# Kernel optimization log

Measured on AMD Instinct MI355X. Metric: run time of the kernel, lower is better.

Reference implementation:

```python
import jax, jax.numpy as jnp
from jax import lax
import numpy as np

HID = 64      # lstm hidden / gat in-dim
HEADS = 4
DH = HID // HEADS  # 16 per-head dim
OUT = 3       # horizon


def setup_inputs() -> dict:
    key = jax.random.key(0)
    ks = jax.random.split(key, 18)
    B, T, N = 8, 12, 1500
    p = lambda k, shape: jax.random.normal(k, shape, jnp.float32) * 0.1
    return {
        "x": jax.random.normal(ks[0], (B, T, N), jnp.float32),
        "adj": jax.random.randint(ks[1], (N, N), 0, 2, jnp.int32),
        "lstm_Wih0": p(ks[2], (4 * HID, 1)),
        "lstm_Whh0": p(ks[3], (4 * HID, HID)),
        "lstm_bih0": p(ks[4], (4 * HID,)),
        "lstm_bhh0": p(ks[5], (4 * HID,)),
        "lstm_Wih1": p(ks[6], (4 * HID, HID)),
        "lstm_Whh1": p(ks[7], (4 * HID, HID)),
        "lstm_bih1": p(ks[8], (4 * HID,)),
        "lstm_bhh1": p(ks[9], (4 * HID,)),
        "gat0_W": p(ks[10], (HID, HID)),
        "gat0_asrc": p(ks[11], (HEADS, DH)),
        "gat0_adst": p(ks[12], (HEADS, DH)),
        "gat1_W": p(ks[13], (HID, HID)),
        "gat1_asrc": p(ks[14], (HEADS, DH)),
        "gat1_adst": p(ks[15], (HEADS, DH)),
        "out_W": p(ks[16], (OUT, HID)),
        "out_b": p(ks[17], (OUT,)),
    }


def _lstm_layer(seq, Wih, Whh, bih, bhh):
    # seq: (T, BN, in) -> (T, BN, H). PyTorch gate order i,f,g,o.
    BN = seq.shape[1]
    H = Whh.shape[1]

    def step(carry, xt):
        h, c = carry
        g = xt @ Wih.T + h @ Whh.T + bih + bhh
        i, f, gg, o = jnp.split(g, 4, axis=-1)
        c = jax.nn.sigmoid(f) * c + jax.nn.sigmoid(i) * jnp.tanh(gg)
        h = jax.nn.sigmoid(o) * jnp.tanh(c)
        return (h, c), h

    zero = jnp.zeros((BN, H), seq.dtype)
    _, hs = lax.scan(step, (zero, zero), seq)
    return hs


def _gat(h_in, W, asrc, adst, mask):
    # h_in: (B,N,HID); mask: (1,N,N,1) bool
    B, N, _ = h_in.shape
    Hn, D = asrc.shape
    hp = (h_in @ W.T).reshape(B, N, Hn, D)           # (B,N,H,D)
    e_src = jnp.einsum('bnhd,hd->bnh', hp, asrc)
    e_dst = jnp.einsum('bnhd,hd->bnh', hp, adst)
    e = e_src[:, :, None, :] + e_dst[:, None, :, :]   # (B,i,j,H)
    e = jnp.where(e > 0, e, 0.2 * e)                  # LeakyReLU(0.2)
    e = jnp.where(mask, e, -jnp.inf)
    alpha = jax.nn.softmax(e, axis=2)                 # softmax over neighbors j
    ho = jnp.einsum('bijh,bjhd->bihd', alpha, hp)
    return ho.reshape(B, N, Hn * D)


def reference(x, adj, lstm_Wih0, lstm_Whh0, lstm_bih0, lstm_bhh0,
              lstm_Wih1, lstm_Whh1, lstm_bih1, lstm_bhh1,
              gat0_W, gat0_asrc, gat0_adst, gat1_W, gat1_asrc, gat1_adst,
              out_W, out_b):
    B, T, N = x.shape
    # (B,T,N) -> (B*N, T, 1) -> time-major (T, B*N, 1)
    xf = jnp.transpose(x, (0, 2, 1)).reshape(B * N, T, 1)
    seq = jnp.transpose(xf, (1, 0, 2))
    hs = _lstm_layer(seq, lstm_Wih0, lstm_Whh0, lstm_bih0, lstm_bhh0)
    hs = _lstm_layer(hs, lstm_Wih1, lstm_Whh1, lstm_bih1, lstm_bhh1)
    h = hs[-1].reshape(B, N, HID)                     # last-step hidden of top layer
    mask = (adj > 0)[None, :, :, None]
    h = jax.nn.relu(_gat(h, gat0_W, gat0_asrc, gat0_adst, mask))
    h = jax.nn.relu(_gat(h, gat1_W, gat1_asrc, gat1_adst, mask))
    out = h @ out_W.T + out_b                         # (B,N,OUT)
    return jnp.transpose(out, (0, 2, 1))              # (B,OUT,N)
```

## Files before the change

### kernel.cpp

```cpp
#include <hip/hip_runtime.h>
#include <hip/hip_bf16.h>


#define BN 12000
#define NNODE 1500
#define NB 8
#define TT 12
#define NPAD 1536
#define LOG2E 1.44269504f

typedef __bf16 bf16x8 __attribute__((ext_vector_type(8)));
typedef __bf16 bf16x4 __attribute__((ext_vector_type(4)));
typedef float  f32x4  __attribute__((ext_vector_type(4)));

__device__ __forceinline__ float rcpf(float v) { return __builtin_amdgcn_rcpf(v); }
__device__ __forceinline__ float exp2f_(float v) { return __builtin_amdgcn_exp2f(v); }
__device__ __forceinline__ float sigf(float v) { return rcpf(1.f + __expf(-v)); }
__device__ __forceinline__ float tanhf_(float v) {
    return fmaf(2.f, rcpf(1.f + __expf(-2.f * v)), -1.f);
}

__device__ __forceinline__ int hp_idx(int b, int head, int jc) {
    return (((b << 2) + head) * 48 + jc) << 9;
}

__device__ __forceinline__ bf16x8 ldcvt(const float* p) {
    f32x4 a = *(const f32x4*)p;
    f32x4 b = *(const f32x4*)(p + 4);
    bf16x8 r;
    #pragma unroll
    for (int i = 0; i < 4; ++i) { r[i] = (__bf16)a[i]; r[4 + i] = (__bf16)b[i]; }
    return r;
}

__global__ __launch_bounds__(512, 1) void lstm_mask_prep(
    const float* __restrict__ x,
    const float* __restrict__ Wih0, const float* __restrict__ Whh0,
    const float* __restrict__ bih0, const float* __restrict__ bhh0,
    const float* __restrict__ Wih1, const float* __restrict__ Whh1,
    const float* __restrict__ bih1, const float* __restrict__ bhh1,
    const int* __restrict__ adj, unsigned int* __restrict__ mask,
    const float* __restrict__ gW, const float* __restrict__ asrc,
    const float* __restrict__ adst,
    __bf16* __restrict__ hpT, float* __restrict__ esT, float* __restrict__ edT)
{
    if (blockIdx.x >= 750) {
        int wid  = (blockIdx.x - 750) * 8 + (threadIdx.x >> 6);
        int lane = threadIdx.x & 63;
        #pragma unroll 4
        for (int u = 0; u < 16; ++u) {
            int task = wid * 16 + u;
            int i = task / 24, ch = task - i * 24;
            int j = ch * 64 + lane;
            int a = (i < NNODE && j < NNODE) ? adj[i * NNODE + j] : 0;
            unsigned long long m = __ballot(a > 0);
            if (lane == 0 && i < 1504) *(unsigned long long*)&mask[i * 48 + ch * 2] = m;
        }
        return;
    }

    __shared__ __align__(16) __bf16 h0s[16 * 72];
    __shared__ __align__(16) __bf16 h1s[16 * 72];
    __shared__ __align__(16) float  xls[TT * 16];
    __shared__ float avs[128];
    __shared__ __align__(16) __bf16 hp_t[64 * 24];

    int tid  = threadIdx.x;
    int w    = __builtin_amdgcn_readfirstlane(tid >> 6);
    int lane = tid & 63;
    int l15  = lane & 15;
    int qd   = lane >> 4;
    bool lo  = l15 < 8;
    int dloc = l15 & 7;
    int d    = 8 * w + dloc;

    for (int e = tid; e < (16 * 72) / 2; e += 512) ((unsigned int*)h1s)[e] = 0u;
    if (tid < TT * 16) {
        int t = tid >> 4, m = tid & 15;
        int s = blockIdx.x * 16 + m;
        int bb = s / NNODE, nn = s - bb * NNODE;
        xls[tid] = x[bb * (TT * NNODE) + t * NNODE + nn];
    }
    if (tid < 64)       avs[tid] = asrc[tid] * LOG2E;
    else if (tid < 128) avs[tid] = adst[tid - 64] * LOG2E;

    int gA = (lo ? 0 : 64) + d;
    int gB = (lo ? 128 : 192) + d;
    bf16x8 B0A[2], B0B[2], B1A[4], B1B[4];
    #pragma unroll
    for (int kt = 0; kt < 2; ++kt) {
        B0A[kt] = ldcvt(&Whh0[gA * 64 + 32 * kt + 8 * qd]);
        B0B[kt] = ldcvt(&Whh0[gB * 64 + 32 * kt + 8 * qd]);
        B1A[kt] = ldcvt(&Wih1[gA * 64 + 32 * kt + 8 * qd]);
        B1B[kt] = ldcvt(&Wih1[gB * 64 + 32 * kt + 8 * qd]);
        B1A[kt + 2] = ldcvt(&Whh1[gA * 64 + 32 * kt + 8 * qd]);
        B1B[kt + 2] = ldcvt(&Whh1[gB * 64 + 32 * kt + 8 * qd]);
    }
    float b0A = bih0[gA] + bhh0[gA], b0B = bih0[gB] + bhh0[gB];
    float b1A = bih1[gA] + bhh1[gA], b1B = bih1[gB] + bhh1[gB];
    float w0A = Wih0[gA], w0B = Wih0[gB];

    float pwi = Wih0[d],       pbi = bih0[d]       + bhh0[d];
    float pwg = Wih0[128 + d], pbg = bih0[128 + d] + bhh0[128 + d];
    float pwo = Wih0[192 + d], pbo = bih0[192 + d] + bhh0[192 + d];

    float c0[2], c1[2];
    c0[0] = c0[1] = c1[0] = c1[1] = 0.f;

    __syncthreads();

    #pragma unroll
    for (int rl = 0; rl < 2; ++rl) {
        int rr = lo ? rl : 2 + rl;
        int m = 4 * qd + rr;
        float xv = xls[m];
        float gi = fmaf(pwi, xv, pbi);
        float gg = fmaf(pwg, xv, pbg);
        float go = fmaf(pwo, xv, pbo);
        float c = sigf(gi) * tanhf_(gg);
        c0[rl] = c;
        h0s[m * 72 + d] = (__bf16)(sigf(go) * tanhf_(c));
    }
    __syncthreads();

    for (int t = 0; t < TT; ++t) {
        bool last = (t == TT - 1);
        bf16x8 a0[2], a1[2];
        #pragma unroll
        for (int kt = 0; kt < 2; ++kt) {
            a0[kt] = *(bf16x8*)&h0s[l15 * 72 + 32 * kt + 8 * qd];
            a1[kt] = *(bf16x8*)&h1s[l15 * 72 + 32 * kt + 8 * qd];
        }
        f32x4 AA1, AB1, AA0, AB0;
        #pragma unroll
        for (int r = 0; r < 4; ++r) { AA1[r] = b1A; AB1[r] = b1B; }
        if (!last) {
            f32x4 xv = *(f32x4*)&xls[(t + 1) * 16 + 4 * qd];
            #pragma unroll
            for (int r = 0; r < 4; ++r) {
                AA0[r] = fmaf(w0A, xv[r], b0A);
                AB0[r] = fmaf(w0B, xv[r], b0B);
            }
        }
        #pragma unroll
        for (int kt = 0; kt < 2; ++kt) {
            AA1 = __builtin_amdgcn_mfma_f32_16x16x32_bf16(a0[kt], B1A[kt], AA1, 0, 0, 0);
            AB1 = __builtin_amdgcn_mfma_f32_16x16x32_bf16(a0[kt], B1B[kt], AB1, 0, 0, 0);
            AA1 = __builtin_amdgcn_mfma_f32_16x16x32_bf16(a1[kt], B1A[kt + 2], AA1, 0, 0, 0);
            AB1 = __builtin_amdgcn_mfma_f32_16x16x32_bf16(a1[kt], B1B[kt + 2], AB1, 0, 0, 0);
        }
        if (!last) {
            #pragma unroll
            for (int kt = 0; kt < 2; ++kt) {
                AA0 = __builtin_amdgcn_mfma_f32_16x16x32_bf16(a0[kt], B0A[kt], AA0, 0, 0, 0);
                AB0 = __builtin_amdgcn_mfma_f32_16x16x32_bf16(a0[kt], B0B[kt], AB0, 0, 0, 0);
            }
        }
        __syncthreads();

        {
            float shA0 = __shfl_xor(lo ? AA1[2] : AA1[0], 8);
            float shA1 = __shfl_xor(lo ? AA1[3] : AA1[1], 8);
            float shB0 = __shfl_xor(lo ? AB1[2] : AB1[0], 8);
            float shB1 = __shfl_xor(lo ? AB1[3] : AB1[1], 8);
            #pragma unroll
            for (int rl = 0; rl < 2; ++rl) {
                int rr = lo ? rl : 2 + rl;
                float ownA = AA1[rr], ownB = AB1[rr];
                float shA = rl ? shA1 : shA0, shB = rl ? shB1 : shB0;
                float gi = lo ? ownA : shA;
                float gf = lo ? shA : ownA;
                float gg = lo ? ownB : shB;
                float go = lo ? shB : ownB;
                float c = sigf(gf) * c1[rl] + sigf(gi) * tanhf_(gg);
                c1[rl] = c;
                float hv = sigf(go) * tanhf_(c);
                int m = 4 * qd + rr;
                h1s[m * 72 + d] = (__bf16)hv;
            }
        }
        if (!last) {
            float shA0 = __shfl_xor(lo ? AA0[2] : AA0[0], 8);
            float shA1 = __shfl_xor(lo ? AA0[3] : AA0[1], 8);
            float shB0 = __shfl_xor(lo ? AB0[2] : AB0[0], 8);
            float shB1 = __shfl_xor(lo ? AB0[3] : AB0[1], 8);
            #pragma unroll
            for (int rl = 0; rl < 2; ++rl) {
                int rr = lo ? rl : 2 + rl;
                float ownA = AA0[rr], ownB = AB0[rr];
                float shA = rl ? shA1 : shA0, shB = rl ? shB1 : shB0;
                float gi = lo ? ownA : shA;
                float gf = lo ? shA : ownA;
                float gg = lo ? ownB : shB;
                float go = lo ? shB : ownB;
                float c = sigf(gf) * c0[rl] + sigf(gi) * tanhf_(gg);
                c0[rl] = c;
                int m = 4 * qd + rr;
                h0s[m * 72 + d] = (__bf16)(sigf(go) * tanhf_(c));
            }
        }
        __syncthreads();
    }

    int s0 = blockIdx.x * 16;
    if (w < 4) {
        int mt = w;
        bf16x8 Bf0 = *(bf16x8*)&h1s[l15 * 72 + 8 * qd];
        bf16x8 Bf1 = *(bf16x8*)&h1s[l15 * 72 + 32 + 8 * qd];
        bf16x8 A0 = ldcvt(&gW[(mt * 16 + l15) * 64 + 8 * qd]);
        bf16x8 A1 = ldcvt(&gW[(mt * 16 + l15) * 64 + 32 + 8 * qd]);
        f32x4 a = {0.f, 0.f, 0.f, 0.f};
        a = __builtin_amdgcn_mfma_f32_16x16x32_bf16(A0, Bf0, a, 0, 0, 0);
        a = __builtin_amdgcn_mfma_f32_16x16x32_bf16(A1, Bf1, a, 0, 0, 0);
        float ts = 0.f, td = 0.f;
        #pragma unroll
        for (int r = 0; r < 4; ++r) {
            int dd = mt * 16 + qd * 4 + r;
            ts = fmaf(a[r], avs[dd], ts);
            td = fmaf(a[r], avs[64 + dd], td);
            hp_t[dd * 24 + l15] = (__bf16)a[r];
        }
        ts += __shfl_xor(ts, 16); ts += __shfl_xor(ts, 32);
        td += __shfl_xor(td, 16); td += __shfl_xor(td, 32);
        if (qd == 0) {
            int s = s0 + l15, b = s / NNODE, n = s - b * NNODE;
            esT[(b * 4 + mt) * NPAD + n] = ts;
            edT[(b * 4 + mt) * NPAD + n] = td;
        }
    }
    __syncthreads();
    if (tid < 256) {
        int dim = tid >> 2, seg = tid & 3;
        int head = dim >> 4, dl = dim & 15;
        int b0 = s0 / NNODE, b1e = (s0 + 15) / NNODE;
        if (b0 == b1e) {
            int n0 = s0 - b0 * NNODE;
            int nj = n0 + seg * 4;
            int jc = nj >> 5, ko = nj & 31;
            bf16x4 v = *(bf16x4*)&hp_t[dim * 24 + seg * 4];
            *(bf16x4*)&hpT[hp_idx(b0, head, jc) + dl * 32 + ko] = v;
        } else {
            #pragma unroll
            for (int u = 0; u < 4; ++u) {
                int ss = s0 + seg * 4 + u;
                int b = ss / NNODE, n = ss - b * NNODE;
                hpT[hp_idx(b, head, n >> 5) + dl * 32 + (n & 31)] =
                    hp_t[dim * 24 + seg * 4 + u];
            }
        }
    }
}

__global__ __launch_bounds__(256, 1) void gat_mid(
    const __bf16* __restrict__ hpT, const float* __restrict__ esT,
    const float* __restrict__ edT, const unsigned int* __restrict__ mask,
    const float* __restrict__ gW, const float* __restrict__ asrc,
    const float* __restrict__ adst,
    __bf16* __restrict__ hpT1, float* __restrict__ esT1, float* __restrict__ edT1)
{
    __shared__ __align__(16) float edls[4 * NPAD];
    __shared__ unsigned int mskls[48 * 16];
    __shared__ float Ss[4][16];
    __shared__ float hbuf[16 * 72];
    __shared__ float avs[128];
    __shared__ __align__(16) __bf16 hp1_t[64 * 24];

    int tid  = threadIdx.x;
    int wv   = tid >> 6;
    int lane = tid & 63;
    int l15  = lane & 15;
    int qd   = lane >> 4;
    int b    = blockIdx.x / 94;
    int i0   = (blockIdx.x % 94) * 16;

    if (tid < 64)       avs[tid] = asrc[tid] * LOG2E;
    else if (tid < 128) avs[tid] = adst[tid - 64] * LOG2E;
    {
        const float4* src = (const float4*)(edT + (b * 4) * NPAD);
        float4* dst = (float4*)edls;
        for (int u = tid; u < NPAD; u += 256) dst[u] = src[u];
    }
    for (int u = tid; u < 16 * 48; u += 256) {
        int il = u / 48, c = u - il * 48;
        mskls[c * 16 + il] = mask[(i0 + il) * 48 + c];
    }
    __syncthreads();

    const __bf16* Bbase = hpT + hp_idx(b, wv, 0) + l15 * 32 + qd * 8;
    const float* edrow = edls + wv * NPAD;
    float esv = esT[(b * 4 + wv) * NPAD + i0 + l15];

    f32x4 acc = {0.f, 0.f, 0.f, 0.f};
    float S = 0.f;

    for (int jt = 0; jt < 12; ++jt) {
        #pragma unroll
        for (int kt = 0; kt < 4; ++kt) {
            int jc = jt * 4 + kt;
            int jk = jc * 32 + qd * 8;
            float4 e0 = *(const float4*)&edrow[jk];
            float4 e1 = *(const float4*)&edrow[jk + 4];
            unsigned int mb = (mskls[jc * 16 + l15] >> (qd * 8)) & 0xffu;
            float ej[8] = {e0.x, e0.y, e0.z, e0.w, e1.x, e1.y, e1.z, e1.w};
            bf16x8 A;
            #pragma unroll
            for (int jj = 0; jj < 8; ++jj) {
                float e = esv + ej[jj];
                e = fmaxf(e, 0.2f * e);
                float p = ((mb >> jj) & 1u) ? exp2f_(e) : 0.f;
                S += p;
                A[jj] = (__bf16)p;
            }
            bf16x8 B = *(const bf16x8*)(Bbase + (jc << 9));
            acc = __builtin_amdgcn_mfma_f32_16x16x32_bf16(A, B, acc, 0, 0, 0);
        }
    }

    S += __shfl_xor(S, 16);
    S += __shfl_xor(S, 32);
    if (qd == 0) Ss[wv][l15] = S;
    __syncthreads();

    #pragma unroll
    for (int r = 0; r < 4; ++r) {
        float rs = rcpf(Ss[wv][qd * 4 + r]);
        hbuf[(qd * 4 + r) * 72 + (wv << 4) + l15] = fmaxf(acc[r] * rs, 0.f);
    }
    __syncthreads();

    {
        int mt = wv;
        bf16x8 Bf0 = ldcvt(&hbuf[l15 * 72 + 8 * qd]);
        bf16x8 Bf1 = ldcvt(&hbuf[l15 * 72 + 32 + 8 * qd]);
        bf16x8 A0 = ldcvt(&gW[(mt * 16 + l15) * 64 + 8 * qd]);
        bf16x8 A1 = ldcvt(&gW[(mt * 16 + l15) * 64 + 32 + 8 * qd]);
        f32x4 a = {0.f, 0.f, 0.f, 0.f};
        a = __builtin_amdgcn_mfma_f32_16x16x32_bf16(A0, Bf0, a, 0, 0, 0);
        a = __builtin_amdgcn_mfma_f32_16x16x32_bf16(A1, Bf1, a, 0, 0, 0);
        float ts = 0.f, td = 0.f;
        #pragma unroll
        for (int r = 0; r < 4; ++r) {
            int dd = mt * 16 + qd * 4 + r;
            ts = fmaf(a[r], avs[dd], ts);
            td = fmaf(a[r], avs[64 + dd], td);
            hp1_t[dd * 24 + l15] = (__bf16)a[r];
        }
        ts += __shfl_xor(ts, 16); ts += __shfl_xor(ts, 32);
        td += __shfl_xor(td, 16); td += __shfl_xor(td, 32);
        if (qd == 0) {
            int n = i0 + l15;
            esT1[(b * 4 + mt) * NPAD + n] = ts;
            edT1[(b * 4 + mt) * NPAD + n] = td;
        }
    }
    __syncthreads();
    {
        int dim = tid >> 2, seg = tid & 3;
        int head = dim >> 4, dl = dim & 15;
        int nn0 = i0 + seg * 4;
        int jc = nn0 >> 5, ko = nn0 & 31;
        bf16x4 v = *(bf16x4*)&hp1_t[dim * 24 + seg * 4];
        *(bf16x4*)&hpT1[hp_idx(b, head, jc) + dl * 32 + ko] = v;
    }
}

__global__ __launch_bounds__(256, 1) void gat_fin(
    const __bf16* __restrict__ hpT, const float* __restrict__ esT,
    const float* __restrict__ edT, const unsigned int* __restrict__ mask,
    const float* __restrict__ oW, const float* __restrict__ ob,
    float* __restrict__ outp)
{
    __shared__ __align__(16) float edls[4 * NPAD];
    __shared__ unsigned int mskls[48 * 16];
    __shared__ float Ss[4][16];
    __shared__ float hbuf[16 * 72];
    __shared__ float oWs[192];
    __shared__ float obs[3];

    int tid  = threadIdx.x;
    int wv   = tid >> 6;
    int lane = tid & 63;
    int l15  = lane & 15;
    int qd   = lane >> 4;
    int b    = blockIdx.x / 94;
    int i0   = (blockIdx.x % 94) * 16;

    if (tid < 192) oWs[tid] = oW[tid];
    if (tid < 3)   obs[tid] = ob[tid];
    {
        const float4* src = (const float4*)(edT + (b * 4) * NPAD);
        float4* dst = (float4*)edls;
        for (int u = tid; u < NPAD; u += 256) dst[u] = src[u];
    }
    for (int u = tid; u < 16 * 48; u += 256) {
        int il = u / 48, c = u - il * 48;
        mskls[c * 16 + il] = mask[(i0 + il) * 48 + c];
    }
    __syncthreads();

    const __bf16* Bbase = hpT + hp_idx(b, wv, 0) + l15 * 32 + qd * 8;
    const float* edrow = edls + wv * NPAD;
    float esv = esT[(b * 4 + wv) * NPAD + i0 + l15];

    f32x4 acc = {0.f, 0.f, 0.f, 0.f};
    float S = 0.f;

    for (int jt = 0; jt < 12; ++jt) {
        #pragma unroll
        for (int kt = 0; kt < 4; ++kt) {
            int jc = jt * 4 + kt;
            int jk = jc * 32 + qd * 8;
            float4 e0 = *(const float4*)&edrow[jk];
            float4 e1 = *(const float4*)&edrow[jk + 4];
            unsigned int mb = (mskls[jc * 16 + l15] >> (qd * 8)) & 0xffu;
            float ej[8] = {e0.x, e0.y, e0.z, e0.w, e1.x, e1.y, e1.z, e1.w};
            bf16x8 A;
            #pragma unroll
            for (int jj = 0; jj < 8; ++jj) {
                float e = esv + ej[jj];
                e = fmaxf(e, 0.2f * e);
                float p = ((mb >> jj) & 1u) ? exp2f_(e) : 0.f;
                S += p;
                A[jj] = (__bf16)p;
            }
            bf16x8 B = *(const bf16x8*)(Bbase + (jc << 9));
            acc = __builtin_amdgcn_mfma_f32_16x16x32_bf16(A, B, acc, 0, 0, 0);
        }
    }

    S += __shfl_xor(S, 16);
    S += __shfl_xor(S, 32);
    if (qd == 0) Ss[wv][l15] = S;
    __syncthreads();

    #pragma unroll
    for (int r = 0; r < 4; ++r) {
        float rs = rcpf(Ss[wv][qd * 4 + r]);
        hbuf[(qd * 4 + r) * 72 + (wv << 4) + l15] = fmaxf(acc[r] * rs, 0.f);
    }
    __syncthreads();

    if (tid < 192) {
        int idx = tid >> 2, ks = tid & 3;
        int nl = idx & 15, o = idx >> 4;
        if (i0 + nl < NNODE) {
            const float* hb = &hbuf[nl * 72 + ks * 16];
            float a = 0.f;
            #pragma unroll
            for (int kk = 0; kk < 16; ++kk)
                a = fmaf(hb[kk], oWs[o * 64 + ks * 16 + kk], a);
            a += __shfl_xor(a, 1);
            a += __shfl_xor(a, 2);
            if (ks == 0)
                outp[(long)b * 3 * NNODE + o * NNODE + i0 + nl] = a + obs[o];
        }
    }
}

extern "C" void kernel_launch(void* const* d_in, const int* in_sizes, int n_in,
                              void* d_out, int out_size, void* d_ws, size_t ws_size,
                              hipStream_t stream) {
    const float* x    = (const float*)d_in[0];
    const int*   adj  = (const int*)d_in[1];
    const float* Wih0 = (const float*)d_in[2];
    const float* Whh0 = (const float*)d_in[3];
    const float* bih0 = (const float*)d_in[4];
    const float* bhh0 = (const float*)d_in[5];
    const float* Wih1 = (const float*)d_in[6];
    const float* Whh1 = (const float*)d_in[7];
    const float* bih1 = (const float*)d_in[8];
    const float* bhh1 = (const float*)d_in[9];
    const float* g0W  = (const float*)d_in[10];
    const float* g0s  = (const float*)d_in[11];
    const float* g0d  = (const float*)d_in[12];
    const float* g1W  = (const float*)d_in[13];
    const float* g1s  = (const float*)d_in[14];
    const float* g1d  = (const float*)d_in[15];
    const float* oW   = (const float*)d_in[16];
    const float* ob   = (const float*)d_in[17];

    float* ws = (float*)d_ws;
    float*        esT0  = ws;
    float*        edT0  = ws + 49152;
    float*        esT1  = ws + 98304;
    float*        edT1  = ws + 147456;
    __bf16*       hpT0  = (__bf16*)(ws + 196608);
    __bf16*       hpT1  = (__bf16*)(ws + 589824);
    unsigned int* maskp = (unsigned int*)(ws + 983040);

    lstm_mask_prep<<<1032, 512, 0, stream>>>(x, Wih0, Whh0, bih0, bhh0,
                                             Wih1, Whh1, bih1, bhh1,
                                             adj, maskp, g0W, g0s, g0d,
                                             hpT0, esT0, edT0);
    gat_mid<<<752, 256, 0, stream>>>(hpT0, esT0, edT0, maskp,
                                     g1W, g1s, g1d, hpT1, esT1, edT1);
    gat_fin<<<752, 256, 0, stream>>>(hpT1, esT1, edT1, maskp,
                                     oW, ob, (float*)d_out);
}
```

Measured before the change: 200.9 us.

## Split GAT neighbor loop across two wave groups with 512-thread blocks

Both GAT kernels now launch 512 threads per block, and each head's neighbor range is split into two halves handled by different waves. Partial accumulators and softmax sums from the second half are passed through shared memory and combined before normalization. The intent is to raise wave-level parallelism and halve the serial length of the exp/MFMA loop. The cost is extra LDS traffic, an extra reduction step, and some threads sitting idle in the epilogue.

```diff
diff --git a/kernel.cpp b/kernel.cpp
--- a/kernel.cpp
+++ b/kernel.cpp
@@ -251,7 +251,7 @@
     }
 }
 
-__global__ __launch_bounds__(256, 1) void gat_mid(
+__global__ __launch_bounds__(512, 1) void gat_mid(
     const __bf16* __restrict__ hpT, const float* __restrict__ esT,
     const float* __restrict__ edT, const unsigned int* __restrict__ mask,
     const float* __restrict__ gW, const float* __restrict__ asrc,
@@ -260,7 +260,8 @@
 {
     __shared__ __align__(16) float edls[4 * NPAD];
     __shared__ unsigned int mskls[48 * 16];
-    __shared__ float Ss[4][16];
+    __shared__ float Ss[8][16];
+    __shared__ __align__(16) f32x4 accs[256];
     __shared__ float hbuf[16 * 72];
     __shared__ float avs[128];
     __shared__ __align__(16) __bf16 hp1_t[64 * 24];
@@ -270,6 +271,8 @@
     int lane = tid & 63;
     int l15  = lane & 15;
     int qd   = lane >> 4;
+    int hh   = wv & 3;
+    int jh   = wv >> 2;
     int b    = blockIdx.x / 94;
     int i0   = (blockIdx.x % 94) * 16;
 
@@ -278,25 +281,26 @@
     {
         const float4* src = (const float4*)(edT + (b * 4) * NPAD);
         float4* dst = (float4*)edls;
-        for (int u = tid; u < NPAD; u += 256) dst[u] = src[u];
-    }
-    for (int u = tid; u < 16 * 48; u += 256) {
+        for (int u = tid; u < NPAD; u += 512) dst[u] = src[u];
+    }
+    for (int u = tid; u < 16 * 48; u += 512) {
         int il = u / 48, c = u - il * 48;
         mskls[c * 16 + il] = mask[(i0 + il) * 48 + c];
     }
     __syncthreads();
 
-    const __bf16* Bbase = hpT + hp_idx(b, wv, 0) + l15 * 32 + qd * 8;
-    const float* edrow = edls + wv * NPAD;
-    float esv = esT[(b * 4 + wv) * NPAD + i0 + l15];
+    const __bf16* Bbase = hpT + hp_idx(b, hh, 0) + l15 * 32 + qd * 8;
+    const float* edrow = edls + hh * NPAD;
+    float esv = esT[(b * 4 + hh) * NPAD + i0 + l15];
 
     f32x4 acc = {0.f, 0.f, 0.f, 0.f};
     float S = 0.f;
 
-    for (int jt = 0; jt < 12; ++jt) {
+    int jc0 = jh * 24;
+    for (int jt = 0; jt < 6; ++jt) {
         #pragma unroll
         for (int kt = 0; kt < 4; ++kt) {
-            int jc = jt * 4 + kt;
+            int jc = jc0 + jt * 4 + kt;
             int jk = jc * 32 + qd * 8;
             float4 e0 = *(const float4*)&edrow[jk];
             float4 e1 = *(const float4*)&edrow[jk + 4];
@@ -319,17 +323,23 @@
     S += __shfl_xor(S, 16);
     S += __shfl_xor(S, 32);
     if (qd == 0) Ss[wv][l15] = S;
-    __syncthreads();
-
-    #pragma unroll
-    for (int r = 0; r < 4; ++r) {
-        float rs = rcpf(Ss[wv][qd * 4 + r]);
-        hbuf[(qd * 4 + r) * 72 + (wv << 4) + l15] = fmaxf(acc[r] * rs, 0.f);
-    }
-    __syncthreads();
-
-    {
-        int mt = wv;
+    if (jh == 1) accs[hh * 64 + lane] = acc;
+    __syncthreads();
+
+    if (jh == 0) {
+        f32x4 o = accs[hh * 64 + lane];
+        #pragma unroll
+        for (int r = 0; r < 4; ++r) {
+            float st = Ss[hh][qd * 4 + r] + Ss[4 + hh][qd * 4 + r];
+            float rs = rcpf(st);
+            hbuf[(qd * 4 + r) * 72 + (hh << 4) + l15] =
+                fmaxf((acc[r] + o[r]) * rs, 0.f);
+        }
+    }
+    __syncthreads();
+
+    if (jh == 0) {
+        int mt = hh;
         bf16x8 Bf0 = ldcvt(&hbuf[l15 * 72 + 8 * qd]);
         bf16x8 Bf1 = ldcvt(&hbuf[l15 * 72 + 32 + 8 * qd]);
         bf16x8 A0 = ldcvt(&gW[(mt * 16 + l15) * 64 + 8 * qd]);
@@ -354,7 +364,7 @@
         }
     }
     __syncthreads();
-    {
+    if (tid < 256) {
         int dim = tid >> 2, seg = tid & 3;
         int head = dim >> 4, dl = dim & 15;
         int nn0 = i0 + seg * 4;
@@ -364,7 +374,7 @@
     }
 }
 
-__global__ __launch_bounds__(256, 1) void gat_fin(
+__global__ __launch_bounds__(512, 1) void gat_fin(
     const __bf16* __restrict__ hpT, const float* __restrict__ esT,
     const float* __restrict__ edT, const unsigned int* __restrict__ mask,
     const float* __restrict__ oW, const float* __restrict__ ob,
@@ -372,7 +382,8 @@
 {
     __shared__ __align__(16) float edls[4 * NPAD];
     __shared__ unsigned int mskls[48 * 16];
-    __shared__ float Ss[4][16];
+    __shared__ float Ss[8][16];
+    __shared__ __align__(16) f32x4 accs[256];
     __shared__ float hbuf[16 * 72];
     __shared__ float oWs[192];
     __shared__ float obs[3];
@@ -382,6 +393,8 @@
     int lane = tid & 63;
     int l15  = lane & 15;
     int qd   = lane >> 4;
+    int hh   = wv & 3;
+    int jh   = wv >> 2;
     int b    = blockIdx.x / 94;
     int i0   = (blockIdx.x % 94) * 16;
 
@@ -390,25 +403,26 @@
     {
         const float4* src = (const float4*)(edT + (b * 4) * NPAD);
         float4* dst = (float4*)edls;
-        for (int u = tid; u < NPAD; u += 256) dst[u] = src[u];
-    }
-    for (int u = tid; u < 16 * 48; u += 256) {
+        for (int u = tid; u < NPAD; u += 512) dst[u] = src[u];
+    }
+    for (int u = tid; u < 16 * 48; u += 512) {
         int il = u / 48, c = u - il * 48;
         mskls[c * 16 + il] = mask[(i0 + il) * 48 + c];
     }
     __syncthreads();
 
-    const __bf16* Bbase = hpT + hp_idx(b, wv, 0) + l15 * 32 + qd * 8;
-    const float* edrow = edls + wv * NPAD;
-    float esv = esT[(b * 4 + wv) * NPAD + i0 + l15];
+    const __bf16* Bbase = hpT + hp_idx(b, hh, 0) + l15 * 32 + qd * 8;
+    const float* edrow = edls + hh * NPAD;
+    float esv = esT[(b * 4 + hh) * NPAD + i0 + l15];
 
     f32x4 acc = {0.f, 0.f, 0.f, 0.f};
     float S = 0.f;
 
-    for (int jt = 0; jt < 12; ++jt) {
+    int jc0 = jh * 24;
+    for (int jt = 0; jt < 6; ++jt) {
         #pragma unroll
         for (int kt = 0; kt < 4; ++kt) {
-            int jc = jt * 4 + kt;
+            int jc = jc0 + jt * 4 + kt;
             int jk = jc * 32 + qd * 8;
             float4 e0 = *(const float4*)&edrow[jk];
             float4 e1 = *(const float4*)&edrow[jk + 4];
@@ -431,12 +445,18 @@
     S += __shfl_xor(S, 16);
     S += __shfl_xor(S, 32);
     if (qd == 0) Ss[wv][l15] = S;
-    __syncthreads();
-
-    #pragma unroll
-    for (int r = 0; r < 4; ++r) {
-        float rs = rcpf(Ss[wv][qd * 4 + r]);
-        hbuf[(qd * 4 + r) * 72 + (wv << 4) + l15] = fmaxf(acc[r] * rs, 0.f);
+    if (jh == 1) accs[hh * 64 + lane] = acc;
+    __syncthreads();
+
+    if (jh == 0) {
+        f32x4 o = accs[hh * 64 + lane];
+        #pragma unroll
+        for (int r = 0; r < 4; ++r) {
+            float st = Ss[hh][qd * 4 + r] + Ss[4 + hh][qd * 4 + r];
+            float rs = rcpf(st);
+            hbuf[(qd * 4 + r) * 72 + (hh << 4) + l15] =
+                fmaxf((acc[r] + o[r]) * rs, 0.f);
+        }
     }
     __syncthreads();
 
@@ -492,8 +512,8 @@
                                              Wih1, Whh1, bih1, bhh1,
                                              adj, maskp, g0W, g0s, g0d,
                                              hpT0, esT0, edT0);
-    gat_mid<<<752, 256, 0, stream>>>(hpT0, esT0, edT0, maskp,
+    gat_mid<<<752, 512, 0, stream>>>(hpT0, esT0, edT0, maskp,
                                      g1W, g1s, g1d, hpT1, esT1, edT1);
-    gat_fin<<<752, 256, 0, stream>>>(hpT1, esT1, edT1, maskp,
+    gat_fin<<<752, 512, 0, stream>>>(hpT1, esT1, edT1, maskp,
                                      oW, ob, (float*)d_out);
 }
```

New measurement: 190.6 us. 5.2% less time.
